# Performance work log

Measured on AMD Instinct MI355X. Metric: run time of the kernel, lower is better.

Reference implementation:

```python
import jax, jax.numpy as jnp
import numpy as np

B, T, D, H, O = 8, 16384, 256, 256, 256


def setup_inputs() -> dict:
    key = jax.random.key(0)
    ks = jax.random.split(key, 7)
    lim_d = 1.0 / np.sqrt(D)
    lim_h = 1.0 / np.sqrt(H)
    u = lambda k, shape, lim: jax.random.uniform(k, shape, jnp.float32, -lim, lim)
    return {
        "xs": jax.random.normal(ks[0], (B, T, D), jnp.float32),
        "Wz": u(ks[1], (H, D), lim_d),
        "bz": u(ks[2], (H,), lim_d),
        "Wh": u(ks[3], (H, D), lim_d),
        "bh": u(ks[4], (H,), lim_d),
        "Wo": u(ks[5], (O, H), lim_h),
        "bo": u(ks[6], (O,), lim_h),
    }


def reference(xs, Wz, bz, Wh, bh, Wo, bo):
    # gates and candidate hidden states (eqx.nn.Linear: y = W @ x + b)
    zs = jax.nn.sigmoid(jnp.einsum("btd,hd->bth", xs, Wz) + bz)  # [B,T,H]
    hs = jnp.einsum("btd,hd->bth", xs, Wh) + bh                  # [B,T,H]

    # prepend_ones / prepend_zeros along the time axis
    a = jnp.concatenate([jnp.ones_like(zs[:, :1]), 1.0 - zs], axis=1)    # [B,T+1,H]
    b = jnp.concatenate([jnp.zeros_like(zs[:, :1]), zs * hs], axis=1)    # [B,T+1,H]

    def combine(first, second):
        a0, b0 = first
        a1, b1 = second
        return (a0 * b0, b0 * a1 + b1)

    _, states = jax.lax.associative_scan(combine, (a, b), axis=1)
    return jnp.einsum("bth,oh->bto", states[:, 1:], Wo) + bo  # [B,T,O]
```

## Files before the change

### kernel.cpp

```cpp
#include <hip/hip_runtime.h>
#include <hip/hip_bf16.h>

#define Bsz 8
#define Tsz 16384
#define NL0 16385
#define NL5 512
#define NL10 16

typedef __attribute__((ext_vector_type(2))) float f32x2;
typedef __attribute__((ext_vector_type(4))) float f32x4;
typedef __attribute__((ext_vector_type(8))) short bf16x8;

__device__ __forceinline__ short f2bf(float f) {
  unsigned u = __builtin_bit_cast(unsigned, f);
  u += 0x7FFFu + ((u >> 16) & 1u);
  return (short)(u >> 16);
}
__device__ __forceinline__ unsigned cvtpk(float lo, float hi) {
  __hip_bfloat162 t = __float22bfloat162_rn(float2{lo, hi});
  unsigned u;
  __builtin_memcpy(&u, &t, 4);
  return u;
}
__device__ __forceinline__ bf16x8 pack8(f32x4 a, f32x4 b) {
  union { unsigned u[4]; bf16x8 v; } r;
  r.u[0] = cvtpk(a[0], a[1]); r.u[1] = cvtpk(a[2], a[3]);
  r.u[2] = cvtpk(b[0], b[1]); r.u[3] = cvtpk(b[2], b[3]);
  return r.v;
}
__device__ __forceinline__ void unpk(unsigned u, float& a, float& b) {
  a = __builtin_bit_cast(float, u << 16);
  b = __builtin_bit_cast(float, u & 0xFFFF0000u);
}

__global__ void fill_sentinel(float* __restrict__ out, int n) {
  int i = blockIdx.x * blockDim.x + threadIdx.x;
  if (i < n) out[i] = 12345.0f;
}

__global__ void prep_weights(const float* __restrict__ Wz, const float* __restrict__ Wh,
                             const float* __restrict__ Wo, unsigned short* __restrict__ wt) {
  int idx = blockIdx.x * 256 + threadIdx.x;
  if (idx >= 3 * 256 * 32) return;
  int m   = idx >> 13;
  int rem = idx & 8191;
  int r   = rem >> 5;
  int cq  = rem & 31;
  const float* src = (m == 0 ? Wz : (m == 1 ? Wh : Wo)) + r * 256 + cq * 8;
  f32x4 v0 = *(const f32x4*)src;
  f32x4 v1 = *(const f32x4*)(src + 4);
  *(bf16x8*)(wt + m * 65536 + (cq * 256 + r) * 8) = pack8(v0, v1);
}

__global__ __launch_bounds__(256, 3)
void gemm_zh(const float* __restrict__ xs, const unsigned short* __restrict__ wt,
             const float* __restrict__ bz, const float* __restrict__ bh,
             unsigned* __restrict__ l0, f32x2* __restrict__ l5)
{
  __shared__ __align__(16) unsigned short aL[32][32][8];

  const int tid = threadIdx.x;
  const int wave = tid >> 6, lane = tid & 63, l15 = lane & 15, l4 = lane >> 4;
  const int bid = blockIdx.x;
  const int batch = bid / 513;
  const int cb = bid - batch * 513;
  const unsigned short* wz_t = wt;
  const unsigned short* wh_t = wt + 65536;
  const int wn = wave * 64;

  unsigned* const l0b = l0 + (size_t)batch * (NL0 * 256);
  f32x2* const l5b = l5 + (size_t)batch * (512 * 256);

  {
    const int gr0i = batch * Tsz + 32 * cb - 1;
    const int rowsMax = Bsz * Tsz - 1;
    f32x4 av0[4], av1[4];
#pragma unroll
    for (int k = 0; k < 4; ++k) {
      const int row = (tid >> 5) + k * 8;
      const int col = (tid & 31) * 8;
      int gr = gr0i + row;
      gr = gr < 0 ? 0 : (gr > rowsMax ? rowsMax : gr);
      const float* p = xs + (((unsigned)gr << 8) + (unsigned)col);
      av0[k] = *(const f32x4*)p;
      av1[k] = *(const f32x4*)(p + 4);
    }
#pragma unroll
    for (int k = 0; k < 4; ++k) {
      const int o = tid + k * 256;
      const int row = o >> 5, oct = o & 31;
      *(bf16x8*)&aL[row][oct ^ (row & 7)][0] = pack8(av0[k], av1[k]);
    }
  }
  __syncthreads();

  f32x4 accz[2][4] = {};
  f32x4 acch[2][4] = {};

#pragma unroll
  for (int kk = 0; kk < 8; ++kk) {
    bf16x8 af[2];
#pragma unroll
    for (int m = 0; m < 2; ++m) {
      const int row = m * 16 + l15;
      af[m] = *(const bf16x8*)&aL[row][(kk * 4 + l4) ^ (row & 7)][0];
    }
    const int cq = kk * 4 + l4;
    bf16x8 zf[4], hf[4];
#pragma unroll
    for (int n = 0; n < 4; ++n) {
      const int r = wn + n * 16 + l15;
      zf[n] = *(const bf16x8*)(wz_t + (cq * 256 + r) * 8);
      hf[n] = *(const bf16x8*)(wh_t + (cq * 256 + r) * 8);
    }
#pragma unroll
    for (int m = 0; m < 2; ++m)
#pragma unroll
      for (int n = 0; n < 4; ++n) {
        accz[m][n] = __builtin_amdgcn_mfma_f32_16x16x32_bf16(af[m], zf[n], accz[m][n], 0, 0, 0);
        acch[m][n] = __builtin_amdgcn_mfma_f32_16x16x32_bf16(af[m], hf[n], acch[m][n], 0, 0, 0);
      }
  }

  const unsigned base0 = ((unsigned)(32 * cb) << 8) + (unsigned)(wn + l15) + ((unsigned)l4 << 10);
#pragma unroll
  for (int n = 0; n < 4; ++n) {
    const int col = wn + n * 16 + l15;
    const float bzv = bz[col], bhv = bh[col];
#pragma unroll
    for (int m = 0; m < 2; ++m)
#pragma unroll
      for (int j = 0; j < 4; ++j) {
        const int e = m * 16 + l4 * 4 + j;
        const float zv = __builtin_amdgcn_rcpf(1.0f + __expf(-(accz[m][n][j] + bzv)));
        const float hv = acch[m][n][j] + bhv;
        float a = 1.0f - zv, b = zv * hv;
        if (cb == 0 && e == 0) { a = 1.0f; b = 0.0f; }
        const unsigned u = cvtpk(a, b);
        if (cb < 512 || e == 0)
          l0b[base0 + (unsigned)(n * 16 + m * 4096 + j * 256)] = u;
        float ar, br; unpk(u, ar, br);
        accz[m][n][j] = ar; acch[m][n][j] = br;
      }
  }

  if (cb < 512) {
    const bool f3 = (l4 & 1) == 0;
    const bool f4 = (l4 & 2) == 0;
#pragma unroll
    for (int n = 0; n < 4; ++n) {
      float a4v[2], b4v[2];
#pragma unroll
      for (int m = 0; m < 2; ++m) {
        const float a10 = accz[m][n][0] * acch[m][n][0];
        const float b10 = acch[m][n][0] * accz[m][n][1] + acch[m][n][1];
        const float a11 = accz[m][n][2] * acch[m][n][2];
        const float b11 = acch[m][n][2] * accz[m][n][3] + acch[m][n][3];
        const float a2 = a10 * b10;
        const float b2 = b10 * a11 + b11;
        const float pa = __shfl_xor(a2, 16);
        const float pb = __shfl_xor(b2, 16);
        const float a3 = f3 ? a2 * b2 : pa * pb;
        const float b3 = f3 ? b2 * pa + pb : pb * a2 + b2;
        const float qa = __shfl_xor(a3, 32);
        const float qb = __shfl_xor(b3, 32);
        a4v[m] = f4 ? a3 * b3 : qa * qb;
        b4v[m] = f4 ? b3 * qa + qb : qb * a3 + b3;
      }
      const float a5 = a4v[0] * b4v[0];
      const float b5 = b4v[0] * a4v[1] + b4v[1];
      if (l4 == 0)
        l5b[((unsigned)cb << 8) + (unsigned)(wn + n * 16 + l15)] = f32x2{a5, b5};
    }
  }
}

__global__ __launch_bounds__(256)
void chunk_up(const f32x2* __restrict__ src, f32x2* __restrict__ dst, int nCh, int nSrc)
{
  int idx = blockIdx.x * 256 + threadIdx.x;
  int total = Bsz * nCh * 256;
  if (idx >= total) return;
  int h = idx & 255, r = idx >> 8;
  int c = r % nCh, batch = r / nCh;
  size_t base = ((size_t)batch * nSrc + (size_t)c * 32) * 256 + h;

  float a1[16], b1[16];
#pragma unroll
  for (int i = 0; i < 16; ++i) {
    f32x2 e0 = src[base + (size_t)(2 * i) * 256];
    f32x2 e1 = src[base + (size_t)(2 * i + 1) * 256];
    a1[i] = e0[0] * e0[1];
    b1[i] = e0[1] * e1[0] + e1[1];
  }
#pragma unroll
  for (int n = 8; n >= 1; n >>= 1) {
#pragma unroll
    for (int i = 0; i < n; ++i) {
      float na = a1[2 * i] * b1[2 * i];
      float nb = b1[2 * i] * a1[2 * i + 1] + b1[2 * i + 1];
      a1[i] = na; b1[i] = nb;
    }
  }
  dst[((size_t)batch * nCh + c) * 256 + h] = f32x2{a1[0], b1[0]};
}

__global__ void tree16(const f32x2* __restrict__ src, float* __restrict__ outB)
{
  int idx = blockIdx.x * 256 + threadIdx.x;
  if (idx >= Bsz * 256) return;
  int h = idx & 255, batch = idx >> 8;
  size_t base = (size_t)batch * 16 * 256 + h;

  float a0[16], b0[16];
#pragma unroll
  for (int i = 0; i < 16; ++i) { f32x2 e = src[base + (size_t)i * 256]; a0[i] = e[0]; b0[i] = e[1]; }
  float a1[8], b1[8];
#pragma unroll
  for (int i = 0; i < 8; ++i) { a1[i] = a0[2*i]*b0[2*i]; b1[i] = b0[2*i]*a0[2*i+1] + b0[2*i+1]; }
  float a2[4], b2[4];
#pragma unroll
  for (int i = 0; i < 4; ++i) { a2[i] = a1[2*i]*b1[2*i]; b2[i] = b1[2*i]*a1[2*i+1] + b1[2*i+1]; }
  float a3[2], b3[2];
#pragma unroll
  for (int i = 0; i < 2; ++i) { a3[i] = a2[2*i]*b2[2*i]; b3[i] = b2[2*i]*a2[2*i+1] + b2[2*i+1]; }
  float s3[2];
  s3[0] = b3[0];
  s3[1] = b3[0] * a3[1] + b3[1];
  float s2[4];
  s2[0] = b2[0]; s2[1] = s3[0]; s2[2] = s3[0] * a2[2] + b2[2]; s2[3] = s3[1];
  float s1[8];
  s1[0] = b1[0];
#pragma unroll
  for (int j = 0; j < 4; ++j) s1[2*j+1] = s2[j];
#pragma unroll
  for (int j = 1; j < 4; ++j) s1[2*j] = s2[j-1] * a1[2*j] + b1[2*j];
  float s0[16];
  s0[0] = b0[0];
#pragma unroll
  for (int j = 0; j < 8; ++j) s0[2*j+1] = s1[j];
#pragma unroll
  for (int j = 1; j < 8; ++j) s0[2*j] = s1[j-1] * a0[2*j] + b0[2*j];
#pragma unroll
  for (int i = 0; i < 16; ++i) outB[base + (size_t)i * 256] = s0[i];
}

__global__ __launch_bounds__(256, 2)
void chunk_down_f32(const f32x2* __restrict__ src, const float* __restrict__ snext,
                    float* __restrict__ outF, int nCh, int nFull, int nSrc)
{
  int idx = blockIdx.x * 256 + threadIdx.x;
  int total = Bsz * nCh * 256;
  if (idx >= total) return;
  int h = idx & 255, r = idx >> 8;
  int c = r % nCh, batch = r / nCh;
  size_t base = ((size_t)batch * nSrc + (size_t)c * 32) * 256 + h;
  bool hasP = (c > 0);
  float P = hasP ? snext[((size_t)batch * nFull + (c - 1)) * 256 + h] : 0.0f;
  float S = snext[((size_t)batch * nFull + c) * 256 + h];

  float ae[16], be[16], a1[16], b1[16];
#pragma unroll
  for (int i = 0; i < 16; ++i) {
    f32x2 e0 = src[base + (size_t)(2 * i) * 256];
    f32x2 e1 = src[base + (size_t)(2 * i + 1) * 256];
    ae[i] = e0[0]; be[i] = e0[1];
    a1[i] = e0[0] * e0[1];
    b1[i] = e0[1] * e1[0] + e1[1];
  }
  float a2[8], b2[8];
#pragma unroll
  for (int i = 0; i < 8; ++i) { a2[i] = a1[2*i]*b1[2*i]; b2[i] = b1[2*i]*a1[2*i+1] + b1[2*i+1]; }
  float a3[4], b3[4];
#pragma unroll
  for (int i = 0; i < 4; ++i) { a3[i] = a2[2*i]*b2[2*i]; b3[i] = b2[2*i]*a2[2*i+1] + b2[2*i+1]; }
  float a4[2], b4[2];
#pragma unroll
  for (int i = 0; i < 2; ++i) { a4[i] = a3[2*i]*b3[2*i]; b4[i] = b3[2*i]*a3[2*i+1] + b3[2*i+1]; }

  float s4[2];
  s4[0] = hasP ? P * a4[0] + b4[0] : b4[0];
  s4[1] = S;
  float s3[4];
  s3[0] = hasP ? P * a3[0] + b3[0] : b3[0];
  s3[1] = s4[0]; s3[2] = s4[0] * a3[2] + b3[2]; s3[3] = s4[1];
  float s2[8];
  s2[0] = hasP ? P * a2[0] + b2[0] : b2[0];
#pragma unroll
  for (int j = 0; j < 4; ++j) s2[2*j+1] = s3[j];
#pragma unroll
  for (int j = 1; j < 4; ++j) s2[2*j] = s3[j-1] * a2[2*j] + b2[2*j];
  float s1[16];
  s1[0] = hasP ? P * a1[0] + b1[0] : b1[0];
#pragma unroll
  for (int j = 0; j < 8; ++j) s1[2*j+1] = s2[j];
#pragma unroll
  for (int j = 1; j < 8; ++j) s1[2*j] = s2[j-1] * a1[2*j] + b1[2*j];

  outF[base] = hasP ? P * ae[0] + be[0] : be[0];
#pragma unroll
  for (int j = 0; j < 16; ++j) outF[base + (size_t)(2*j+1) * 256] = s1[j];
#pragma unroll
  for (int j = 1; j < 16; ++j) outF[base + (size_t)(2*j) * 256] = s1[j-1] * ae[j] + be[j];
}

__global__ __launch_bounds__(256, 3)
void down_proj(const unsigned* __restrict__ l0, const float* __restrict__ s5b,
               const unsigned short* __restrict__ wo_t, const float* __restrict__ bo,
               float* __restrict__ out)
{
  __shared__ unsigned short pL[32 * 256];

  const int tid = threadIdx.x;
  const int bc = blockIdx.x;
  const int c = bc % 513;
  const int batch = bc / 513;

  const unsigned* const l0b = l0 + (size_t)batch * (NL0 * 256);
  const float* const s5bb = s5b + (size_t)batch * (512 * 256);
  float* const outb = out + (size_t)batch * (Tsz * 256);

  {
    const int h = tid;
    const unsigned base = ((unsigned)(c * 32) << 8) + (unsigned)h;
    const bool hasP = (c > 0);
    const float P = hasP ? s5bb[((unsigned)(c - 1) << 8) + h] : 0.0f;

    if (c == 512) {
      float a0, b0; unpk(l0b[base], a0, b0);
      pL[h] = (unsigned short)f2bf(P * a0 + b0);
#pragma unroll
      for (int i = 1; i < 32; ++i)
        pL[i * 256 + (h ^ ((i & 7) << 3))] = 0;
    } else {
      const float S = s5bb[((unsigned)c << 8) + h];
      float ae[16], be[16], a1[16], b1[16];
#pragma unroll
      for (int i = 0; i < 16; ++i) {
        unsigned u0 = l0b[base + ((unsigned)(2 * i) << 8)];
        unsigned u1 = l0b[base + ((unsigned)(2 * i + 1) << 8)];
        float a0, b0, a1e, b1e;
        unpk(u0, a0, b0); unpk(u1, a1e, b1e);
        ae[i] = a0; be[i] = b0;
        a1[i] = a0 * b0; b1[i] = b0 * a1e + b1e;
      }
      float a2[8], b2[8];
#pragma unroll
      for (int i = 0; i < 8; ++i) { a2[i] = a1[2*i]*b1[2*i]; b2[i] = b1[2*i]*a1[2*i+1] + b1[2*i+1]; }
      float a3[4], b3[4];
#pragma unroll
      for (int i = 0; i < 4; ++i) { a3[i] = a2[2*i]*b2[2*i]; b3[i] = b2[2*i]*a2[2*i+1] + b2[2*i+1]; }
      float a4[2], b4[2];
#pragma unroll
      for (int i = 0; i < 2; ++i) { a4[i] = a3[2*i]*b3[2*i]; b4[i] = b3[2*i]*a3[2*i+1] + b3[2*i+1]; }

      float s4[2];
      s4[0] = hasP ? P * a4[0] + b4[0] : b4[0];
      s4[1] = S;
      float s3[4];
      s3[0] = hasP ? P * a3[0] + b3[0] : b3[0];
      s3[1] = s4[0]; s3[2] = s4[0] * a3[2] + b3[2]; s3[3] = s4[1];
      float s2[8];
      s2[0] = hasP ? P * a2[0] + b2[0] : b2[0];
#pragma unroll
      for (int j = 0; j < 4; ++j) s2[2*j+1] = s3[j];
#pragma unroll
      for (int j = 1; j < 4; ++j) s2[2*j] = s3[j-1] * a2[2*j] + b2[2*j];
      float s1[16];
      s1[0] = hasP ? P * a1[0] + b1[0] : b1[0];
#pragma unroll
      for (int j = 0; j < 8; ++j) s1[2*j+1] = s2[j];
#pragma unroll
      for (int j = 1; j < 8; ++j) s1[2*j] = s2[j-1] * a1[2*j] + b1[2*j];

      pL[h] = (unsigned short)f2bf(hasP ? P * ae[0] + be[0] : be[0]);
#pragma unroll
      for (int j = 0; j < 16; ++j) {
        const int row = 2 * j + 1;
        pL[row * 256 + (h ^ ((row & 7) << 3))] = (unsigned short)f2bf(s1[j]);
      }
#pragma unroll
      for (int j = 1; j < 16; ++j) {
        const int row = 2 * j;
        pL[row * 256 + (h ^ ((row & 7) << 3))] = (unsigned short)f2bf(s1[j-1] * ae[j] + be[j]);
      }
    }
  }
  __syncthreads();

  const int wave = tid >> 6, lane = tid & 63, l15 = lane & 15, l4 = lane >> 4;
  const int wn = wave * 64;
  f32x4 acc[2][4] = {};
  bf16x8 wc[4], wnx[4];
#pragma unroll
  for (int n = 0; n < 4; ++n)
    wc[n] = *(const bf16x8*)(wo_t + (l4 * 256 + wn + n * 16 + l15) * 8);
#pragma unroll
  for (int kk = 0; kk < 8; ++kk) {
    if (kk < 7) {
#pragma unroll
      for (int n = 0; n < 4; ++n)
        wnx[n] = *(const bf16x8*)(wo_t + (((kk + 1) * 4 + l4) * 256 + wn + n * 16 + l15) * 8);
    }
    bf16x8 af[2];
#pragma unroll
    for (int m = 0; m < 2; ++m) {
      const int row = m * 16 + l15;
      af[m] = *(const bf16x8*)&pL[row * 256 + ((kk * 32 + l4 * 8) ^ ((row & 7) << 3))];
    }
#pragma unroll
    for (int m = 0; m < 2; ++m)
#pragma unroll
      for (int n = 0; n < 4; ++n)
        acc[m][n] = __builtin_amdgcn_mfma_f32_16x16x32_bf16(af[m], wc[n], acc[m][n], 0, 0, 0);
    if (kk < 7) {
      wc[0] = wnx[0]; wc[1] = wnx[1]; wc[2] = wnx[2]; wc[3] = wnx[3];
    }
  }

  const int tBase = 32 * c - 1;
#pragma unroll
  for (int n = 0; n < 4; ++n) {
    const int col = wn + n * 16 + l15;
    const float bv = bo[col];
#pragma unroll
    for (int m = 0; m < 2; ++m)
#pragma unroll
      for (int j = 0; j < 4; ++j) {
        const int t = tBase + m * 16 + l4 * 4 + j;
        if ((unsigned)t < (unsigned)Tsz)
          outb[((unsigned)t << 8) + (unsigned)col] = acc[m][n][j] + bv;
      }
  }
}

extern "C" void kernel_launch(void* const* d_in, const int* in_sizes, int n_in,
                              void* d_out, int out_size, void* d_ws, size_t ws_size,
                              hipStream_t stream)
{
  (void)in_sizes; (void)n_in;
  const float* xs = (const float*)d_in[0];
  const float* Wz = (const float*)d_in[1];
  const float* bz = (const float*)d_in[2];
  const float* Wh = (const float*)d_in[3];
  const float* bh = (const float*)d_in[4];
  const float* Wo = (const float*)d_in[5];
  const float* bo = (const float*)d_in[6];
  float* out = (float*)d_out;

  const size_t n_l0  = (size_t)Bsz * NL0 * 256;
  const size_t n_l5  = (size_t)Bsz * NL5 * 256;
  const size_t n_l10 = (size_t)Bsz * NL10 * 256;

  unsigned* l0    = (unsigned*)d_ws;
  f32x2* l5ab     = (f32x2*)(l0 + n_l0);
  f32x2* l10ab    = l5ab + n_l5;
  float* s10b     = (float*)(l10ab + n_l10);
  float* s5b      = s10b + n_l10;
  unsigned short* wt = (unsigned short*)(s5b + n_l5);

  const size_t need = n_l0 * 4 + n_l5 * 8 + n_l10 * 8 + n_l10 * 4 + n_l5 * 4 + 3 * 65536 * 2;
  if (ws_size < need) {
    fill_sentinel<<<(out_size + 255) / 256, 256, 0, stream>>>(out, out_size);
    return;
  }

  prep_weights<<<96, 256, 0, stream>>>(Wz, Wh, Wo, wt);
  gemm_zh<<<Bsz * 513, 256, 0, stream>>>(xs, wt, bz, bh, l0, l5ab);
  chunk_up<<<(Bsz * 16 * 256) / 256, 256, 0, stream>>>(l5ab, l10ab, 16, NL5);
  tree16<<<8, 256, 0, stream>>>(l10ab, s10b);
  chunk_down_f32<<<(Bsz * 16 * 256) / 256, 256, 0, stream>>>(l5ab, s10b, s5b, 16, 16, NL5);
  down_proj<<<Bsz * 513, 256, 0, stream>>>(l0, s5b, wt + 2 * 65536, bo, out);
}
```

Before: 168.2 us.

## Recompute gate GEMM in down-projection kernel instead of storing per-step coefficients

The first GEMM kernel no longer writes the per-timestep packed (a,b) scan coefficients to global memory; it only produces chunk-level summaries. The down-projection kernel now reloads the xs tile, recomputes the Wz/Wh GEMM and the gate activations into shared memory, then does the local scan and the output GEMM. This trades a roughly 134 MB write plus read of intermediates for a second pass over xs and a duplicated GEMM's worth of MFMA work, and it raises shared memory use per block.

```diff
diff --git a/kernel.cpp b/kernel.cpp
--- a/kernel.cpp
+++ b/kernel.cpp
@@ -3,7 +3,6 @@
 
 #define Bsz 8
 #define Tsz 16384
-#define NL0 16385
 #define NL5 512
 #define NL10 16
 
@@ -53,22 +52,20 @@
 }
 
 __global__ __launch_bounds__(256, 3)
-void gemm_zh(const float* __restrict__ xs, const unsigned short* __restrict__ wt,
+void gemm_l5(const float* __restrict__ xs, const unsigned short* __restrict__ wt,
              const float* __restrict__ bz, const float* __restrict__ bh,
-             unsigned* __restrict__ l0, f32x2* __restrict__ l5)
+             f32x2* __restrict__ l5)
 {
   __shared__ __align__(16) unsigned short aL[32][32][8];
 
   const int tid = threadIdx.x;
   const int wave = tid >> 6, lane = tid & 63, l15 = lane & 15, l4 = lane >> 4;
   const int bid = blockIdx.x;
-  const int batch = bid / 513;
-  const int cb = bid - batch * 513;
+  const int batch = bid >> 9;
+  const int cb = bid & 511;
   const unsigned short* wz_t = wt;
   const unsigned short* wh_t = wt + 65536;
   const int wn = wave * 64;
-
-  unsigned* const l0b = l0 + (size_t)batch * (NL0 * 256);
   f32x2* const l5b = l5 + (size_t)batch * (512 * 256);
 
   {
@@ -122,7 +119,6 @@
       }
   }
 
-  const unsigned base0 = ((unsigned)(32 * cb) << 8) + (unsigned)(wn + l15) + ((unsigned)l4 << 10);
 #pragma unroll
   for (int n = 0; n < 4; ++n) {
     const int col = wn + n * 16 + l15;
@@ -137,14 +133,12 @@
         float a = 1.0f - zv, b = zv * hv;
         if (cb == 0 && e == 0) { a = 1.0f; b = 0.0f; }
         const unsigned u = cvtpk(a, b);
-        if (cb < 512 || e == 0)
-          l0b[base0 + (unsigned)(n * 16 + m * 4096 + j * 256)] = u;
         float ar, br; unpk(u, ar, br);
         accz[m][n][j] = ar; acch[m][n][j] = br;
       }
   }
 
-  if (cb < 512) {
+  {
     const bool f3 = (l4 & 1) == 0;
     const bool f4 = (l4 & 2) == 0;
 #pragma unroll
@@ -305,29 +299,103 @@
 }
 
 __global__ __launch_bounds__(256, 3)
-void down_proj(const unsigned* __restrict__ l0, const float* __restrict__ s5b,
-               const unsigned short* __restrict__ wo_t, const float* __restrict__ bo,
-               float* __restrict__ out)
+void fused_dp(const float* __restrict__ xs, const unsigned short* __restrict__ wt,
+              const float* __restrict__ bz, const float* __restrict__ bh,
+              const float* __restrict__ s5b, const unsigned short* __restrict__ wo_t,
+              const float* __restrict__ bo, float* __restrict__ out)
 {
-  __shared__ unsigned short pL[32 * 256];
+  __shared__ __align__(16) unsigned short aL[32][32][8];
+  __shared__ unsigned abL[32][256];
+  unsigned short* const pL = &aL[0][0][0];
 
   const int tid = threadIdx.x;
+  const int wave = tid >> 6, lane = tid & 63, l15 = lane & 15, l4 = lane >> 4;
   const int bc = blockIdx.x;
-  const int c = bc % 513;
   const int batch = bc / 513;
-
-  const unsigned* const l0b = l0 + (size_t)batch * (NL0 * 256);
+  const int c = bc - batch * 513;
+  const unsigned short* wz_t = wt;
+  const unsigned short* wh_t = wt + 65536;
+  const int wn = wave * 64;
+
   const float* const s5bb = s5b + (size_t)batch * (512 * 256);
   float* const outb = out + (size_t)batch * (Tsz * 256);
 
   {
+    const int gr0i = batch * Tsz + 32 * c - 1;
+    const int rowsMax = Bsz * Tsz - 1;
+    f32x4 av0[4], av1[4];
+#pragma unroll
+    for (int k = 0; k < 4; ++k) {
+      const int row = (tid >> 5) + k * 8;
+      const int col = (tid & 31) * 8;
+      int gr = gr0i + row;
+      gr = gr < 0 ? 0 : (gr > rowsMax ? rowsMax : gr);
+      const float* p = xs + (((unsigned)gr << 8) + (unsigned)col);
+      av0[k] = *(const f32x4*)p;
+      av1[k] = *(const f32x4*)(p + 4);
+    }
+#pragma unroll
+    for (int k = 0; k < 4; ++k) {
+      const int o = tid + k * 256;
+      const int row = o >> 5, oct = o & 31;
+      *(bf16x8*)&aL[row][oct ^ (row & 7)][0] = pack8(av0[k], av1[k]);
+    }
+  }
+  __syncthreads();
+
+  {
+    f32x4 accz[2][4] = {};
+    f32x4 acch[2][4] = {};
+#pragma unroll
+    for (int kk = 0; kk < 8; ++kk) {
+      bf16x8 af[2];
+#pragma unroll
+      for (int m = 0; m < 2; ++m) {
+        const int row = m * 16 + l15;
+        af[m] = *(const bf16x8*)&aL[row][(kk * 4 + l4) ^ (row & 7)][0];
+      }
+      const int cq = kk * 4 + l4;
+      bf16x8 zf[4], hf[4];
+#pragma unroll
+      for (int n = 0; n < 4; ++n) {
+        const int r = wn + n * 16 + l15;
+        zf[n] = *(const bf16x8*)(wz_t + (cq * 256 + r) * 8);
+        hf[n] = *(const bf16x8*)(wh_t + (cq * 256 + r) * 8);
+      }
+#pragma unroll
+      for (int m = 0; m < 2; ++m)
+#pragma unroll
+        for (int n = 0; n < 4; ++n) {
+          accz[m][n] = __builtin_amdgcn_mfma_f32_16x16x32_bf16(af[m], zf[n], accz[m][n], 0, 0, 0);
+          acch[m][n] = __builtin_amdgcn_mfma_f32_16x16x32_bf16(af[m], hf[n], acch[m][n], 0, 0, 0);
+        }
+    }
+#pragma unroll
+    for (int n = 0; n < 4; ++n) {
+      const int col = wn + n * 16 + l15;
+      const float bzv = bz[col], bhv = bh[col];
+#pragma unroll
+      for (int m = 0; m < 2; ++m)
+#pragma unroll
+        for (int j = 0; j < 4; ++j) {
+          const int e = m * 16 + l4 * 4 + j;
+          const float zv = __builtin_amdgcn_rcpf(1.0f + __expf(-(accz[m][n][j] + bzv)));
+          const float hv = acch[m][n][j] + bhv;
+          float a = 1.0f - zv, b = zv * hv;
+          if (c == 0 && e == 0) { a = 1.0f; b = 0.0f; }
+          abL[e][col ^ ((e & 7) << 3)] = cvtpk(a, b);
+        }
+    }
+  }
+  __syncthreads();
+
+  {
     const int h = tid;
-    const unsigned base = ((unsigned)(c * 32) << 8) + (unsigned)h;
     const bool hasP = (c > 0);
     const float P = hasP ? s5bb[((unsigned)(c - 1) << 8) + h] : 0.0f;
 
     if (c == 512) {
-      float a0, b0; unpk(l0b[base], a0, b0);
+      float a0, b0; unpk(abL[0][h], a0, b0);
       pL[h] = (unsigned short)f2bf(P * a0 + b0);
 #pragma unroll
       for (int i = 1; i < 32; ++i)
@@ -337,8 +405,8 @@
       float ae[16], be[16], a1[16], b1[16];
 #pragma unroll
       for (int i = 0; i < 16; ++i) {
-        unsigned u0 = l0b[base + ((unsigned)(2 * i) << 8)];
-        unsigned u1 = l0b[base + ((unsigned)(2 * i + 1) << 8)];
+        unsigned u0 = abL[2 * i][h ^ (((2 * i) & 7) << 3)];
+        unsigned u1 = abL[2 * i + 1][h ^ (((2 * i + 1) & 7) << 3)];
         float a0, b0, a1e, b1e;
         unpk(u0, a0, b0); unpk(u1, a1e, b1e);
         ae[i] = a0; be[i] = b0;
@@ -388,8 +456,6 @@
   }
   __syncthreads();
 
-  const int wave = tid >> 6, lane = tid & 63, l15 = lane & 15, l4 = lane >> 4;
-  const int wn = wave * 64;
   f32x4 acc[2][4] = {};
   bf16x8 wc[4], wnx[4];
 #pragma unroll
@@ -448,27 +514,25 @@
   const float* bo = (const float*)d_in[6];
   float* out = (float*)d_out;
 
-  const size_t n_l0  = (size_t)Bsz * NL0 * 256;
   const size_t n_l5  = (size_t)Bsz * NL5 * 256;
   const size_t n_l10 = (size_t)Bsz * NL10 * 256;
 
-  unsigned* l0    = (unsigned*)d_ws;
-  f32x2* l5ab     = (f32x2*)(l0 + n_l0);
+  f32x2* l5ab     = (f32x2*)d_ws;
   f32x2* l10ab    = l5ab + n_l5;
   float* s10b     = (float*)(l10ab + n_l10);
   float* s5b      = s10b + n_l10;
   unsigned short* wt = (unsigned short*)(s5b + n_l5);
 
-  const size_t need = n_l0 * 4 + n_l5 * 8 + n_l10 * 8 + n_l10 * 4 + n_l5 * 4 + 3 * 65536 * 2;
+  const size_t need = n_l5 * 8 + n_l10 * 8 + n_l10 * 4 + n_l5 * 4 + 3 * 65536 * 2;
   if (ws_size < need) {
     fill_sentinel<<<(out_size + 255) / 256, 256, 0, stream>>>(out, out_size);
     return;
   }
 
   prep_weights<<<96, 256, 0, stream>>>(Wz, Wh, Wo, wt);
-  gemm_zh<<<Bsz * 513, 256, 0, stream>>>(xs, wt, bz, bh, l0, l5ab);
+  gemm_l5<<<Bsz * 512, 256, 0, stream>>>(xs, wt, bz, bh, l5ab);
   chunk_up<<<(Bsz * 16 * 256) / 256, 256, 0, stream>>>(l5ab, l10ab, 16, NL5);
   tree16<<<8, 256, 0, stream>>>(l10ab, s10b);
   chunk_down_f32<<<(Bsz * 16 * 256) / 256, 256, 0, stream>>>(l5ab, s10b, s5b, 16, 16, NL5);
-  down_proj<<<Bsz * 513, 256, 0, stream>>>(l0, s5b, wt + 2 * 65536, bo, out);
-}
+  fused_dp<<<Bsz * 513, 256, 0, stream>>>(xs, wt, bz, bh, s5b, wt + 2 * 65536, bo, out);
+}
```

New measurement: 175.5 us. +4.3%, slower.

## Retile gemm_zh to 64-row tiles with double-buffered K-chunked LDS staging

Applied to the files above, without the earlier changes.

The gate GEMM kernel now processes 64 time rows per block with 512 threads (8 waves, 32 columns each) instead of 32 rows with 256 threads. The activation tile is loaded in four K-chunks of 64 and double-buffered in LDS, so the next chunk's global load overlaps the MFMA work on the current one. Larger tiles halve how often each block re-reads the weights from global memory. The cost is more accumulator registers per wave and fewer, larger blocks, which may reduce occupancy or balance.

```diff
diff --git a/kernel.cpp b/kernel.cpp
--- a/kernel.cpp
+++ b/kernel.cpp
@@ -52,83 +52,77 @@
   *(bf16x8*)(wt + m * 65536 + (cq * 256 + r) * 8) = pack8(v0, v1);
 }
 
-__global__ __launch_bounds__(256, 3)
+__global__ __launch_bounds__(512, 4)
 void gemm_zh(const float* __restrict__ xs, const unsigned short* __restrict__ wt,
              const float* __restrict__ bz, const float* __restrict__ bh,
              unsigned* __restrict__ l0, f32x2* __restrict__ l5)
 {
-  __shared__ __align__(16) unsigned short aL[32][32][8];
+  __shared__ __align__(16) unsigned short aL[2][4096];
 
   const int tid = threadIdx.x;
   const int wave = tid >> 6, lane = tid & 63, l15 = lane & 15, l4 = lane >> 4;
   const int bid = blockIdx.x;
-  const int batch = bid / 513;
-  const int cb = bid - batch * 513;
+  const int batch = bid / 257;
+  const int cb = bid - batch * 257;
   const unsigned short* wz_t = wt;
   const unsigned short* wh_t = wt + 65536;
-  const int wn = wave * 64;
+  const int wn = wave * 32;
 
   unsigned* const l0b = l0 + (size_t)batch * (NL0 * 256);
   f32x2* const l5b = l5 + (size_t)batch * (512 * 256);
 
-  {
-    const int gr0i = batch * Tsz + 32 * cb - 1;
-    const int rowsMax = Bsz * Tsz - 1;
-    f32x4 av0[4], av1[4];
-#pragma unroll
-    for (int k = 0; k < 4; ++k) {
-      const int row = (tid >> 5) + k * 8;
-      const int col = (tid & 31) * 8;
-      int gr = gr0i + row;
-      gr = gr < 0 ? 0 : (gr > rowsMax ? rowsMax : gr);
-      const float* p = xs + (((unsigned)gr << 8) + (unsigned)col);
-      av0[k] = *(const f32x4*)p;
-      av1[k] = *(const f32x4*)(p + 4);
-    }
-#pragma unroll
-    for (int k = 0; k < 4; ++k) {
-      const int o = tid + k * 256;
-      const int row = o >> 5, oct = o & 31;
-      *(bf16x8*)&aL[row][oct ^ (row & 7)][0] = pack8(av0[k], av1[k]);
-    }
-  }
-  __syncthreads();
-
-  f32x4 accz[2][4] = {};
-  f32x4 acch[2][4] = {};
-
-#pragma unroll
-  for (int kk = 0; kk < 8; ++kk) {
-    bf16x8 af[2];
-#pragma unroll
-    for (int m = 0; m < 2; ++m) {
-      const int row = m * 16 + l15;
-      af[m] = *(const bf16x8*)&aL[row][(kk * 4 + l4) ^ (row & 7)][0];
-    }
-    const int cq = kk * 4 + l4;
-    bf16x8 zf[4], hf[4];
-#pragma unroll
-    for (int n = 0; n < 4; ++n) {
-      const int r = wn + n * 16 + l15;
-      zf[n] = *(const bf16x8*)(wz_t + (cq * 256 + r) * 8);
-      hf[n] = *(const bf16x8*)(wh_t + (cq * 256 + r) * 8);
-    }
-#pragma unroll
-    for (int m = 0; m < 2; ++m)
-#pragma unroll
-      for (int n = 0; n < 4; ++n) {
-        accz[m][n] = __builtin_amdgcn_mfma_f32_16x16x32_bf16(af[m], zf[n], accz[m][n], 0, 0, 0);
-        acch[m][n] = __builtin_amdgcn_mfma_f32_16x16x32_bf16(af[m], hf[n], acch[m][n], 0, 0, 0);
-      }
-  }
-
-  const unsigned base0 = ((unsigned)(32 * cb) << 8) + (unsigned)(wn + l15) + ((unsigned)l4 << 10);
-#pragma unroll
-  for (int n = 0; n < 4; ++n) {
+  const int srow = tid & 63, soct = tid >> 6;
+  const int rowsMax = Bsz * Tsz - 1;
+  int gr = batch * Tsz + 64 * cb - 1 + srow;
+  gr = gr < 0 ? 0 : (gr > rowsMax ? rowsMax : gr);
+  const float* aptr = xs + (((unsigned)gr << 8) + (unsigned)(soct * 8));
+
+  f32x4 av0 = *(const f32x4*)(aptr);
+  f32x4 av1 = *(const f32x4*)(aptr + 4);
+  *(bf16x8*)&aL[0][(soct * 64 + srow) * 8] = pack8(av0, av1);
+
+  f32x4 accz[4][2] = {};
+  f32x4 acch[4][2] = {};
+
+  for (int S = 0; S < 4; ++S) {
+    __syncthreads();
+    const int cur = S & 1;
+    if (S < 3) {
+      av0 = *(const f32x4*)(aptr + (S + 1) * 64);
+      av1 = *(const f32x4*)(aptr + (S + 1) * 64 + 4);
+    }
+#pragma unroll
+    for (int k2 = 0; k2 < 2; ++k2) {
+      bf16x8 af[4], zf[2], hf[2];
+#pragma unroll
+      for (int m = 0; m < 4; ++m)
+        af[m] = *(const bf16x8*)&aL[cur][((k2 * 4 + l4) * 64 + m * 16 + l15) * 8];
+      const int cq = (S * 2 + k2) * 4 + l4;
+#pragma unroll
+      for (int n = 0; n < 2; ++n) {
+        const int r = wn + n * 16 + l15;
+        zf[n] = *(const bf16x8*)(wz_t + (cq * 256 + r) * 8);
+        hf[n] = *(const bf16x8*)(wh_t + (cq * 256 + r) * 8);
+      }
+#pragma unroll
+      for (int m = 0; m < 4; ++m)
+#pragma unroll
+        for (int n = 0; n < 2; ++n) {
+          accz[m][n] = __builtin_amdgcn_mfma_f32_16x16x32_bf16(af[m], zf[n], accz[m][n], 0, 0, 0);
+          acch[m][n] = __builtin_amdgcn_mfma_f32_16x16x32_bf16(af[m], hf[n], acch[m][n], 0, 0, 0);
+        }
+    }
+    if (S < 3)
+      *(bf16x8*)&aL[cur ^ 1][(soct * 64 + srow) * 8] = pack8(av0, av1);
+  }
+
+  const unsigned base0 = ((unsigned)(64 * cb) << 8) + (unsigned)(wn + l15) + ((unsigned)l4 << 10);
+#pragma unroll
+  for (int n = 0; n < 2; ++n) {
     const int col = wn + n * 16 + l15;
     const float bzv = bz[col], bhv = bh[col];
 #pragma unroll
-    for (int m = 0; m < 2; ++m)
+    for (int m = 0; m < 4; ++m)
 #pragma unroll
       for (int j = 0; j < 4; ++j) {
         const int e = m * 16 + l4 * 4 + j;
@@ -137,40 +131,44 @@
         float a = 1.0f - zv, b = zv * hv;
         if (cb == 0 && e == 0) { a = 1.0f; b = 0.0f; }
         const unsigned u = cvtpk(a, b);
-        if (cb < 512 || e == 0)
+        if (cb < 256 || e == 0)
           l0b[base0 + (unsigned)(n * 16 + m * 4096 + j * 256)] = u;
         float ar, br; unpk(u, ar, br);
         accz[m][n][j] = ar; acch[m][n][j] = br;
       }
   }
 
-  if (cb < 512) {
+  if (cb < 256) {
     const bool f3 = (l4 & 1) == 0;
     const bool f4 = (l4 & 2) == 0;
 #pragma unroll
-    for (int n = 0; n < 4; ++n) {
-      float a4v[2], b4v[2];
-#pragma unroll
-      for (int m = 0; m < 2; ++m) {
-        const float a10 = accz[m][n][0] * acch[m][n][0];
-        const float b10 = acch[m][n][0] * accz[m][n][1] + acch[m][n][1];
-        const float a11 = accz[m][n][2] * acch[m][n][2];
-        const float b11 = acch[m][n][2] * accz[m][n][3] + acch[m][n][3];
-        const float a2 = a10 * b10;
-        const float b2 = b10 * a11 + b11;
-        const float pa = __shfl_xor(a2, 16);
-        const float pb = __shfl_xor(b2, 16);
-        const float a3 = f3 ? a2 * b2 : pa * pb;
-        const float b3 = f3 ? b2 * pa + pb : pb * a2 + b2;
-        const float qa = __shfl_xor(a3, 32);
-        const float qb = __shfl_xor(b3, 32);
-        a4v[m] = f4 ? a3 * b3 : qa * qb;
-        b4v[m] = f4 ? b3 * qa + qb : qb * a3 + b3;
-      }
-      const float a5 = a4v[0] * b4v[0];
-      const float b5 = b4v[0] * a4v[1] + b4v[1];
-      if (l4 == 0)
-        l5b[((unsigned)cb << 8) + (unsigned)(wn + n * 16 + l15)] = f32x2{a5, b5};
+    for (int n = 0; n < 2; ++n) {
+#pragma unroll
+      for (int half = 0; half < 2; ++half) {
+        float a4v[2], b4v[2];
+#pragma unroll
+        for (int mm = 0; mm < 2; ++mm) {
+          const int m = half * 2 + mm;
+          const float a10 = accz[m][n][0] * acch[m][n][0];
+          const float b10 = acch[m][n][0] * accz[m][n][1] + acch[m][n][1];
+          const float a11 = accz[m][n][2] * acch[m][n][2];
+          const float b11 = acch[m][n][2] * accz[m][n][3] + acch[m][n][3];
+          const float a2 = a10 * b10;
+          const float b2 = b10 * a11 + b11;
+          const float pa = __shfl_xor(a2, 16);
+          const float pb = __shfl_xor(b2, 16);
+          const float a3 = f3 ? a2 * b2 : pa * pb;
+          const float b3 = f3 ? b2 * pa + pb : pb * a2 + b2;
+          const float qa = __shfl_xor(a3, 32);
+          const float qb = __shfl_xor(b3, 32);
+          a4v[mm] = f4 ? a3 * b3 : qa * qb;
+          b4v[mm] = f4 ? b3 * qa + qb : qb * a3 + b3;
+        }
+        const float a5 = a4v[0] * b4v[0];
+        const float b5 = b4v[0] * a4v[1] + b4v[1];
+        if (l4 == 0)
+          l5b[((unsigned)(2 * cb + half) << 8) + (unsigned)(wn + n * 16 + l15)] = f32x2{a5, b5};
+      }
     }
   }
 }
@@ -466,7 +464,7 @@
   }
 
   prep_weights<<<96, 256, 0, stream>>>(Wz, Wh, Wo, wt);
-  gemm_zh<<<Bsz * 513, 256, 0, stream>>>(xs, wt, bz, bh, l0, l5ab);
+  gemm_zh<<<Bsz * 257, 512, 0, stream>>>(xs, wt, bz, bh, l0, l5ab);
   chunk_up<<<(Bsz * 16 * 256) / 256, 256, 0, stream>>>(l5ab, l10ab, 16, NL5);
   tree16<<<8, 256, 0, stream>>>(l10ab, s10b);
   chunk_down_f32<<<(Bsz * 16 * 256) / 256, 256, 0, stream>>>(l5ab, s10b, s5b, 16, 16, NL5);
```

Result: no change. 168.7 us (+0.3%).
